# Kernel tuning notes

Hardware: AMD Instinct MI355X
Metric: run time of the kernel (lower is better)

The kernel has to match this reference:

```python
import jax, jax.numpy as jnp
import numpy as np

DROPOUT_P = 0.2
HEAD_SIZE = 64
EMBED = 1024


def setup_inputs() -> dict:
    key = jax.random.key(0)
    kx, kk, kq, kv = jax.random.split(key, 4)
    B, T = 4, 4096
    x = jax.random.normal(kx, (B, T, EMBED), dtype=jnp.float32)
    # torch Linear(embed, head, bias=False): y = x @ W.T with W [head, embed].
    # We store W_* as [embed, head] so projection is x @ W.
    scale = 1.0 / np.sqrt(EMBED)
    Wk = jax.random.uniform(kk, (EMBED, HEAD_SIZE), jnp.float32, -scale, scale)
    Wq = jax.random.uniform(kq, (EMBED, HEAD_SIZE), jnp.float32, -scale, scale)
    Wv = jax.random.uniform(kv, (EMBED, HEAD_SIZE), jnp.float32, -scale, scale)
    return {"x": x, "Wk": Wk, "Wq": Wq, "Wv": Wv}


def reference(x, Wk, Wq, Wv):
    # Projections: [B,T,E] @ [E,H] -> [B,T,H]
    k = jnp.einsum("bte,eh->bth", x, Wk)
    q = jnp.einsum("bte,eh->bth", x, Wq)
    v = jnp.einsum("bte,eh->bth", x, Wv)
    # Raw scaled scores, NO softmax: [B,T,T]
    w = jnp.einsum("bqh,bkh->bqk", q, k) * (HEAD_SIZE ** -0.5)
    # Dropout (training mode, inverted scaling) with a fixed key.
    keep = jax.random.bernoulli(jax.random.key(42), 1.0 - DROPOUT_P, w.shape)
    w = jnp.where(keep, w / (1.0 - DROPOUT_P), 0.0)
    # Weighted V sum: [B,T,T] @ [B,T,H] -> [B,T,H]
    return jnp.einsum("bqk,bkh->bqh", w, v)
```

## Files before the change

kernel.cpp:

```cpp
#include <hip/hip_runtime.h>


#define TB 4
#define TT 4096
#define TE 1024
#define TH 64
#define COMB_SCALE 0.15625f

typedef __bf16 bf16x8 __attribute__((ext_vector_type(8)));
typedef __bf16 bf16x4 __attribute__((ext_vector_type(4)));
typedef float  f32x4  __attribute__((ext_vector_type(4)));

#define ROTL(x, d) __builtin_amdgcn_alignbit((x), (x), 32u - (d))

__device__ __forceinline__ unsigned tf_bits(unsigned j) {
  const unsigned ks1 = 42u;
  const unsigned ks2 = 0x1BD11BDAu ^ 42u;
  unsigned x0 = 0u, x1 = j + ks1;
#define TF_RND(d) { x0 += x1; x1 = ROTL(x1, (d)); x1 ^= x0; }
  TF_RND(13u) TF_RND(15u) TF_RND(26u) TF_RND(6u)
  x0 += ks1; x1 += ks2 + 1u;
  TF_RND(17u) TF_RND(29u) TF_RND(16u) TF_RND(24u)
  x0 += ks2; x1 += 0u + 2u;
  TF_RND(13u) TF_RND(15u) TF_RND(26u) TF_RND(6u)
  x0 += 0u;  x1 += ks1 + 3u;
  TF_RND(17u) TF_RND(29u) TF_RND(16u) TF_RND(24u)
  x0 += ks1; x1 += ks2 + 4u;
  TF_RND(13u) TF_RND(15u) TF_RND(26u) TF_RND(6u)
  x0 += ks2; x1 += 0u + 5u;
#undef TF_RND
  return x0 ^ x1;
}

__device__ __forceinline__ unsigned tf_keepmask(unsigned j) {
  return tf_bits(j) < 3435974144u ? 0xFFFFFFFFu : 0u;
}

__global__ __launch_bounds__(256)
void prep_wt(const float* __restrict__ Wq, const float* __restrict__ Wk,
             const float* __restrict__ Wv, __bf16* __restrict__ WT)
{
  __shared__ float lds[64][65];
  const int wi = blockIdx.x >> 4;
  const int k0 = (blockIdx.x & 15) * 64;
  const float* W = (wi == 0) ? Wq : ((wi == 1) ? Wk : Wv);
  const int tid = threadIdx.x;
#pragma unroll
  for (int it = 0; it < 16; ++it) {
    const int idx = tid + it * 256;
    lds[idx >> 6][idx & 63] = W[(size_t)(k0 + (idx >> 6)) * TH + (idx & 63)];
  }
  __syncthreads();
#pragma unroll
  for (int it = 0; it < 16; ++it) {
    const int idx = tid + it * 256;
    const int n = idx >> 6, kk = idx & 63;
    WT[(size_t)(wi * TH + n) * TE + k0 + kk] = (__bf16)lds[kk][n];
  }
}

__global__ __launch_bounds__(256)
void proj_mfma(const float* __restrict__ x, const __bf16* __restrict__ WT,
               __bf16* __restrict__ qs, __bf16* __restrict__ ks,
               __bf16* __restrict__ vT)
{
  const int tid = threadIdx.x;
  const int w  = tid >> 6, l = tid & 63;
  const int l4 = l >> 4,  lm = l & 15;
  const int rh = w >> 1,  ch = w & 1;
  const int R  = blockIdx.x * 32 + rh * 16;

  const float*  xr = x  + (size_t)(R + lm) * TE;
  const __bf16* wt = WT + (size_t)(ch * 96 + lm) * TE;

  f32x4 acc[6];
#pragma unroll
  for (int t = 0; t < 6; ++t) acc[t] = (f32x4){0.f, 0.f, 0.f, 0.f};

  for (int k0 = 0; k0 < TE; k0 += 32) {
    const float4 u0 = *reinterpret_cast<const float4*>(xr + k0 + l4 * 8);
    const float4 u1 = *reinterpret_cast<const float4*>(xr + k0 + l4 * 8 + 4);
    bf16x8 am;
    am[0] = (__bf16)u0.x; am[1] = (__bf16)u0.y;
    am[2] = (__bf16)u0.z; am[3] = (__bf16)u0.w;
    am[4] = (__bf16)u1.x; am[5] = (__bf16)u1.y;
    am[6] = (__bf16)u1.z; am[7] = (__bf16)u1.w;
    bf16x8 bn[6];
#pragma unroll
    for (int t = 0; t < 6; ++t)
      bn[t] = *reinterpret_cast<const bf16x8*>(wt + (size_t)t * 16 * TE + k0 + l4 * 8);
#pragma unroll
    for (int t = 0; t < 6; ++t)
      acc[t] = __builtin_amdgcn_mfma_f32_16x16x32_bf16(am, bn[t], acc[t], 0, 0, 0);
  }

  const int row0 = R + l4 * 4;
#pragma unroll
  for (int t = 0; t < 6; ++t) {
    const int n = ch * 96 + t * 16 + lm;
    if (n < TH) {
#pragma unroll
      for (int r = 0; r < 4; ++r)
        qs[(size_t)(row0 + r) * TH + n] = (__bf16)(acc[t][r] * COMB_SCALE);
    } else if (n < 2 * TH) {
#pragma unroll
      for (int r = 0; r < 4; ++r)
        ks[(size_t)(row0 + r) * TH + (n - TH)] = (__bf16)acc[t][r];
    } else {
      bf16x4 vv;
#pragma unroll
      for (int r = 0; r < 4; ++r) vv[r] = (__bf16)acc[t][r];
      const int bb = row0 >> 12, trow = row0 & (TT - 1);
      *reinterpret_cast<bf16x4*>(
          vT + ((size_t)(bb * TH + (n - 2 * TH)) * TT + trow)) = vv;
    }
  }
}

__global__ __launch_bounds__(256, 4)
void attn_mfma(const __bf16* __restrict__ qs,
               const __bf16* __restrict__ ks,
               const __bf16* __restrict__ vT,
               float* __restrict__ out)
{
  __shared__ __bf16 S_lds[4][16 * 64];
  __shared__ float  Oex[3][16][TH + 4];

  const int tid = threadIdx.x;
  const int w   = tid >> 6;
  const int l   = tid & 63;
  const int l4  = l >> 4;
  const int lm  = l & 15;

  const int b     = blockIdx.x >> 8;
  const int qt16  = blockIdx.x & 255;
  const int qrow0 = qt16 * 16;
  const int kv0   = w * (TT / 4);

  const __bf16* qb = qs + ((size_t)b * TT + qrow0) * TH;
  const bf16x8 qf0 = *reinterpret_cast<const bf16x8*>(qb + (size_t)lm * TH + l4 * 8);
  const bf16x8 qf1 = *reinterpret_cast<const bf16x8*>(qb + (size_t)lm * TH + 32 + l4 * 8);

  const __bf16* kbp = ks + (size_t)b * TT * TH;
  const __bf16* vbp = vT + (size_t)b * TH * TT;

  f32x4 o_acc[4];
#pragma unroll
  for (int t = 0; t < 4; ++t) o_acc[t] = (f32x4){0.f, 0.f, 0.f, 0.f};

  const unsigned base0 = ((unsigned)(b * TT) + (unsigned)qrow0 + (unsigned)(l4 * 4)) * (unsigned)TT;
  const unsigned sw = (unsigned)((lm & 7) << 3);

  for (int kb = kv0; kb < kv0 + TT / 4; kb += 64) {
    bf16x8 kf[4][2];
#pragma unroll
    for (int t = 0; t < 4; ++t) {
      const __bf16* kr = kbp + (size_t)(kb + t * 16 + lm) * TH;
#pragma unroll
      for (int ss = 0; ss < 2; ++ss)
        kf[t][ss] = *reinterpret_cast<const bf16x8*>(kr + ss * 32 + l4 * 8);
    }
    bf16x8 vf[4][2];
#pragma unroll
    for (int t = 0; t < 4; ++t) {
      const __bf16* vr = vbp + (size_t)(t * 16 + lm) * TT + kb;
#pragma unroll
      for (int ss = 0; ss < 2; ++ss)
        vf[t][ss] = *reinterpret_cast<const bf16x8*>(vr + ss * 32 + l4 * 8);
    }

    unsigned km[4][4];
    const unsigned jcol = (unsigned)kb + (unsigned)lm;
#pragma unroll
    for (int t = 0; t < 4; ++t)
#pragma unroll
      for (int r = 0; r < 4; ++r)
        km[t][r] = tf_keepmask(base0 + (unsigned)(r << 12) + jcol + (unsigned)(t << 4));

    f32x4 sa[4];
#pragma unroll
    for (int t = 0; t < 4; ++t) {
      f32x4 c = {0.f, 0.f, 0.f, 0.f};
      c = __builtin_amdgcn_mfma_f32_16x16x32_bf16(qf0, kf[t][0], c, 0, 0, 0);
      c = __builtin_amdgcn_mfma_f32_16x16x32_bf16(qf1, kf[t][1], c, 0, 0, 0);
      sa[t] = c;
    }

#pragma unroll
    for (int t = 0; t < 4; ++t) {
#pragma unroll
      for (int r = 0; r < 4; ++r) {
        const unsigned sb = __float_as_uint(sa[t][r]) & km[t][r];
        const int row = l4 * 4 + r;
        const int col = t * 16 + lm;
        S_lds[w][row * 64 + (col ^ ((row & 7) << 3))] =
            (__bf16)__uint_as_float(sb);
      }
    }

    const bf16x8 af0 = *reinterpret_cast<const bf16x8*>(
        &S_lds[w][lm * 64 + ((unsigned)(l4 * 8) ^ sw)]);
    const bf16x8 af1 = *reinterpret_cast<const bf16x8*>(
        &S_lds[w][lm * 64 + ((unsigned)(32 + l4 * 8) ^ sw)]);

#pragma unroll
    for (int t = 0; t < 4; ++t) {
      o_acc[t] = __builtin_amdgcn_mfma_f32_16x16x32_bf16(af0, vf[t][0], o_acc[t], 0, 0, 0);
      o_acc[t] = __builtin_amdgcn_mfma_f32_16x16x32_bf16(af1, vf[t][1], o_acc[t], 0, 0, 0);
    }
  }

  if (w > 0) {
#pragma unroll
    for (int t = 0; t < 4; ++t)
#pragma unroll
      for (int r = 0; r < 4; ++r)
        Oex[w - 1][l4 * 4 + r][t * 16 + lm] = o_acc[t][r];
  }
  __syncthreads();
  if (w == 0) {
    float* outb = out + ((size_t)b * TT + qrow0) * TH;
#pragma unroll
    for (int t = 0; t < 4; ++t)
#pragma unroll
      for (int r = 0; r < 4; ++r) {
        const int row = l4 * 4 + r, col = t * 16 + lm;
        outb[(size_t)row * TH + col] = o_acc[t][r] + Oex[0][row][col] +
                                       Oex[1][row][col] + Oex[2][row][col];
      }
  }
}

extern "C" void kernel_launch(void* const* d_in, const int* in_sizes, int n_in,
                              void* d_out, int out_size, void* d_ws, size_t ws_size,
                              hipStream_t stream) {
  const float* x  = (const float*)d_in[0];
  const float* Wk = (const float*)d_in[1];
  const float* Wq = (const float*)d_in[2];
  const float* Wv = (const float*)d_in[3];
  float* outp = (float*)d_out;

  const size_t SZ = (size_t)TB * TT * TH;
  __bf16* q_ws  = (__bf16*)d_ws;
  __bf16* k_ws  = q_ws + SZ;
  __bf16* vT_ws = k_ws + SZ;
  __bf16* WT_ws = vT_ws + SZ;

  prep_wt<<<dim3(48), dim3(256), 0, stream>>>(Wq, Wk, Wv, WT_ws);
  proj_mfma<<<dim3(TB * TT / 32), dim3(256), 0, stream>>>(
      x, WT_ws, q_ws, k_ws, vT_ws);
  attn_mfma<<<dim3(TB * (TT / 16)), dim3(256), 0, stream>>>(
      q_ws, k_ws, vT_ws, outp);
}
```

Measured before the change: 203.1 us.

## Double-buffer K/V register loads in attention and prefetch in projection kernel

The attention kernel now ping-pongs between two register sets of K and V fragments, loading the next 64-key tile while the current one is processed, so global-load latency overlaps with the dropout hashing and MFMA work. The projection kernel is regridded to 16 rows per block with each of the four waves owning 48 output columns, which doubles the block count. It also software-prefetches the next x and W slice into registers. The gain in latency hiding costs more live registers, which under launch_bounds(256,4) could cause spills or lower occupancy.

```diff
diff --git a/kernel.cpp b/kernel.cpp
--- a/kernel.cpp
+++ b/kernel.cpp
@@ -32,10 +32,6 @@
   return x0 ^ x1;
 }
 
-__device__ __forceinline__ unsigned tf_keepmask(unsigned j) {
-  return tf_bits(j) < 3435974144u ? 0xFFFFFFFFu : 0u;
-}
-
 __global__ __launch_bounds__(256)
 void prep_wt(const float* __restrict__ Wq, const float* __restrict__ Wk,
              const float* __restrict__ Wv, __bf16* __restrict__ WT)
@@ -67,37 +63,49 @@
   const int tid = threadIdx.x;
   const int w  = tid >> 6, l = tid & 63;
   const int l4 = l >> 4,  lm = l & 15;
-  const int rh = w >> 1,  ch = w & 1;
-  const int R  = blockIdx.x * 32 + rh * 16;
+  const int R  = blockIdx.x * 16;
 
   const float*  xr = x  + (size_t)(R + lm) * TE;
-  const __bf16* wt = WT + (size_t)(ch * 96 + lm) * TE;
-
-  f32x4 acc[6];
-#pragma unroll
-  for (int t = 0; t < 6; ++t) acc[t] = (f32x4){0.f, 0.f, 0.f, 0.f};
+  const __bf16* wt = WT + (size_t)(w * 48 + lm) * TE;
+
+  f32x4 acc[3];
+#pragma unroll
+  for (int t = 0; t < 3; ++t) acc[t] = (f32x4){0.f, 0.f, 0.f, 0.f};
+
+  float4 u0 = *reinterpret_cast<const float4*>(xr + l4 * 8);
+  float4 u1 = *reinterpret_cast<const float4*>(xr + l4 * 8 + 4);
+  bf16x8 bnc[3];
+#pragma unroll
+  for (int t = 0; t < 3; ++t)
+    bnc[t] = *reinterpret_cast<const bf16x8*>(wt + (size_t)t * 16 * TE + l4 * 8);
 
   for (int k0 = 0; k0 < TE; k0 += 32) {
-    const float4 u0 = *reinterpret_cast<const float4*>(xr + k0 + l4 * 8);
-    const float4 u1 = *reinterpret_cast<const float4*>(xr + k0 + l4 * 8 + 4);
+    const int kp = (k0 + 32 < TE) ? (k0 + 32) : 0;
+    const float4 n0 = *reinterpret_cast<const float4*>(xr + kp + l4 * 8);
+    const float4 n1 = *reinterpret_cast<const float4*>(xr + kp + l4 * 8 + 4);
+    bf16x8 bnn[3];
+#pragma unroll
+    for (int t = 0; t < 3; ++t)
+      bnn[t] = *reinterpret_cast<const bf16x8*>(wt + (size_t)t * 16 * TE + kp + l4 * 8);
+
     bf16x8 am;
     am[0] = (__bf16)u0.x; am[1] = (__bf16)u0.y;
     am[2] = (__bf16)u0.z; am[3] = (__bf16)u0.w;
     am[4] = (__bf16)u1.x; am[5] = (__bf16)u1.y;
     am[6] = (__bf16)u1.z; am[7] = (__bf16)u1.w;
-    bf16x8 bn[6];
-#pragma unroll
-    for (int t = 0; t < 6; ++t)
-      bn[t] = *reinterpret_cast<const bf16x8*>(wt + (size_t)t * 16 * TE + k0 + l4 * 8);
-#pragma unroll
-    for (int t = 0; t < 6; ++t)
-      acc[t] = __builtin_amdgcn_mfma_f32_16x16x32_bf16(am, bn[t], acc[t], 0, 0, 0);
+#pragma unroll
+    for (int t = 0; t < 3; ++t)
+      acc[t] = __builtin_amdgcn_mfma_f32_16x16x32_bf16(am, bnc[t], acc[t], 0, 0, 0);
+
+    u0 = n0; u1 = n1;
+#pragma unroll
+    for (int t = 0; t < 3; ++t) bnc[t] = bnn[t];
   }
 
   const int row0 = R + l4 * 4;
 #pragma unroll
-  for (int t = 0; t < 6; ++t) {
-    const int n = ch * 96 + t * 16 + lm;
+  for (int t = 0; t < 3; ++t) {
+    const int n = w * 48 + t * 16 + lm;
     if (n < TH) {
 #pragma unroll
       for (int r = 0; r < 4; ++r)
@@ -151,8 +159,9 @@
   const unsigned base0 = ((unsigned)(b * TT) + (unsigned)qrow0 + (unsigned)(l4 * 4)) * (unsigned)TT;
   const unsigned sw = (unsigned)((lm & 7) << 3);
 
-  for (int kb = kv0; kb < kv0 + TT / 4; kb += 64) {
-    bf16x8 kf[4][2];
+  bf16x8 kfA[4][2], vfA[4][2], kfB[4][2], vfB[4][2];
+
+  auto loadkv = [&](bf16x8 (&kf)[4][2], bf16x8 (&vf)[4][2], int kb) {
 #pragma unroll
     for (int t = 0; t < 4; ++t) {
       const __bf16* kr = kbp + (size_t)(kb + t * 16 + lm) * TH;
@@ -160,7 +169,6 @@
       for (int ss = 0; ss < 2; ++ss)
         kf[t][ss] = *reinterpret_cast<const bf16x8*>(kr + ss * 32 + l4 * 8);
     }
-    bf16x8 vf[4][2];
 #pragma unroll
     for (int t = 0; t < 4; ++t) {
       const __bf16* vr = vbp + (size_t)(t * 16 + lm) * TT + kb;
@@ -168,14 +176,17 @@
       for (int ss = 0; ss < 2; ++ss)
         vf[t][ss] = *reinterpret_cast<const bf16x8*>(vr + ss * 32 + l4 * 8);
     }
-
+  };
+
+  auto work = [&](bf16x8 (&kf)[4][2], bf16x8 (&vf)[4][2], int kb) {
     unsigned km[4][4];
-    const unsigned jcol = (unsigned)kb + (unsigned)lm;
+    const unsigned j00 = base0 + (unsigned)kb + (unsigned)lm;
 #pragma unroll
     for (int t = 0; t < 4; ++t)
 #pragma unroll
       for (int r = 0; r < 4; ++r)
-        km[t][r] = tf_keepmask(base0 + (unsigned)(r << 12) + jcol + (unsigned)(t << 4));
+        km[t][r] = (tf_bits(j00 + (unsigned)((r << 12) + (t << 4))) <
+                    3435974144u) ? 0xFFFFFFFFu : 0u;
 
     f32x4 sa[4];
 #pragma unroll
@@ -208,6 +219,15 @@
       o_acc[t] = __builtin_amdgcn_mfma_f32_16x16x32_bf16(af0, vf[t][0], o_acc[t], 0, 0, 0);
       o_acc[t] = __builtin_amdgcn_mfma_f32_16x16x32_bf16(af1, vf[t][1], o_acc[t], 0, 0, 0);
     }
+  };
+
+  loadkv(kfA, vfA, kv0);
+#pragma unroll
+  for (int s = 0; s < 16; s += 2) {
+    loadkv(kfB, vfB, kv0 + (s + 1) * 64);
+    work(kfA, vfA, kv0 + s * 64);
+    if (s + 2 < 16) loadkv(kfA, vfA, kv0 + (s + 2) * 64);
+    work(kfB, vfB, kv0 + (s + 1) * 64);
   }
 
   if (w > 0) {
@@ -247,7 +267,7 @@
   __bf16* WT_ws = vT_ws + SZ;
 
   prep_wt<<<dim3(48), dim3(256), 0, stream>>>(Wq, Wk, Wv, WT_ws);
-  proj_mfma<<<dim3(TB * TT / 32), dim3(256), 0, stream>>>(
+  proj_mfma<<<dim3(TB * TT / 16), dim3(256), 0, stream>>>(
       x, WT_ws, q_ws, k_ws, vT_ws);
   attn_mfma<<<dim3(TB * (TT / 16)), dim3(256), 0, stream>>>(
       q_ws, k_ws, vT_ws, outp);
```

After: 262.2 us. 29.1% more time.

## Split projection K-dimension across waves with LDS reduction; raise MFMA wave priority

Applied to the files above, without the earlier changes.

The projection kernel now gives each block 16 rows and has each of its four waves cover a quarter of the embedding dimension for all 192 output columns. Partial sums are reduced through a large LDS buffer, which doubles the grid and fully unrolls a shorter K loop. The aim is more parallelism and better latency hiding for the x stream. Separately, the attention kernel raises wave priority around its MFMA sections with s_setprio so matrix work is scheduled ahead of the dropout hash ALU work of other waves. The costs are more LDS (about 50KB per block, which limits occupancy), higher register pressure, and an extra barrier.

```diff
diff --git a/kernel.cpp b/kernel.cpp
--- a/kernel.cpp
+++ b/kernel.cpp
@@ -59,25 +59,26 @@
   }
 }
 
-__global__ __launch_bounds__(256)
+__global__ __launch_bounds__(256, 3)
 void proj_mfma(const float* __restrict__ x, const __bf16* __restrict__ WT,
                __bf16* __restrict__ qs, __bf16* __restrict__ ks,
                __bf16* __restrict__ vT)
 {
+  __shared__ float red[4][16][196];
   const int tid = threadIdx.x;
   const int w  = tid >> 6, l = tid & 63;
   const int l4 = l >> 4,  lm = l & 15;
-  const int rh = w >> 1,  ch = w & 1;
-  const int R  = blockIdx.x * 32 + rh * 16;
-
-  const float*  xr = x  + (size_t)(R + lm) * TE;
-  const __bf16* wt = WT + (size_t)(ch * 96 + lm) * TE;
-
-  f32x4 acc[6];
-#pragma unroll
-  for (int t = 0; t < 6; ++t) acc[t] = (f32x4){0.f, 0.f, 0.f, 0.f};
-
-  for (int k0 = 0; k0 < TE; k0 += 32) {
+  const int R  = blockIdx.x * 16;
+
+  const float*  xr = x  + (size_t)(R + lm) * TE + w * 256;
+  const __bf16* wt = WT + (size_t)lm * TE + w * 256;
+
+  f32x4 acc[12];
+#pragma unroll
+  for (int t = 0; t < 12; ++t) acc[t] = (f32x4){0.f, 0.f, 0.f, 0.f};
+
+#pragma unroll
+  for (int k0 = 0; k0 < 256; k0 += 32) {
     const float4 u0 = *reinterpret_cast<const float4*>(xr + k0 + l4 * 8);
     const float4 u1 = *reinterpret_cast<const float4*>(xr + k0 + l4 * 8 + 4);
     bf16x8 am;
@@ -85,31 +86,44 @@
     am[2] = (__bf16)u0.z; am[3] = (__bf16)u0.w;
     am[4] = (__bf16)u1.x; am[5] = (__bf16)u1.y;
     am[6] = (__bf16)u1.z; am[7] = (__bf16)u1.w;
-    bf16x8 bn[6];
-#pragma unroll
-    for (int t = 0; t < 6; ++t)
+    bf16x8 bn[12];
+#pragma unroll
+    for (int t = 0; t < 12; ++t)
       bn[t] = *reinterpret_cast<const bf16x8*>(wt + (size_t)t * 16 * TE + k0 + l4 * 8);
 #pragma unroll
-    for (int t = 0; t < 6; ++t)
+    for (int t = 0; t < 12; ++t)
       acc[t] = __builtin_amdgcn_mfma_f32_16x16x32_bf16(am, bn[t], acc[t], 0, 0, 0);
   }
 
+#pragma unroll
+  for (int t = 0; t < 12; ++t)
+#pragma unroll
+    for (int r = 0; r < 4; ++r)
+      red[w][l4 * 4 + r][t * 16 + lm] = acc[t][r];
+  __syncthreads();
+
   const int row0 = R + l4 * 4;
 #pragma unroll
-  for (int t = 0; t < 6; ++t) {
-    const int n = ch * 96 + t * 16 + lm;
+  for (int t2 = 0; t2 < 3; ++t2) {
+    const int n = w * 48 + t2 * 16 + lm;
+    float v[4];
+#pragma unroll
+    for (int r = 0; r < 4; ++r) {
+      const int rr = l4 * 4 + r;
+      v[r] = red[0][rr][n] + red[1][rr][n] + red[2][rr][n] + red[3][rr][n];
+    }
     if (n < TH) {
 #pragma unroll
       for (int r = 0; r < 4; ++r)
-        qs[(size_t)(row0 + r) * TH + n] = (__bf16)(acc[t][r] * COMB_SCALE);
+        qs[(size_t)(row0 + r) * TH + n] = (__bf16)(v[r] * COMB_SCALE);
     } else if (n < 2 * TH) {
 #pragma unroll
       for (int r = 0; r < 4; ++r)
-        ks[(size_t)(row0 + r) * TH + (n - TH)] = (__bf16)acc[t][r];
+        ks[(size_t)(row0 + r) * TH + (n - TH)] = (__bf16)v[r];
     } else {
       bf16x4 vv;
 #pragma unroll
-      for (int r = 0; r < 4; ++r) vv[r] = (__bf16)acc[t][r];
+      for (int r = 0; r < 4; ++r) vv[r] = (__bf16)v[r];
       const int bb = row0 >> 12, trow = row0 & (TT - 1);
       *reinterpret_cast<bf16x4*>(
           vT + ((size_t)(bb * TH + (n - 2 * TH)) * TT + trow)) = vv;
@@ -177,6 +191,7 @@
       for (int r = 0; r < 4; ++r)
         km[t][r] = tf_keepmask(base0 + (unsigned)(r << 12) + jcol + (unsigned)(t << 4));
 
+    __builtin_amdgcn_s_setprio(1);
     f32x4 sa[4];
 #pragma unroll
     for (int t = 0; t < 4; ++t) {
@@ -185,6 +200,7 @@
       c = __builtin_amdgcn_mfma_f32_16x16x32_bf16(qf1, kf[t][1], c, 0, 0, 0);
       sa[t] = c;
     }
+    __builtin_amdgcn_s_setprio(0);
 
 #pragma unroll
     for (int t = 0; t < 4; ++t) {
@@ -203,11 +219,13 @@
     const bf16x8 af1 = *reinterpret_cast<const bf16x8*>(
         &S_lds[w][lm * 64 + ((unsigned)(32 + l4 * 8) ^ sw)]);
 
+    __builtin_amdgcn_s_setprio(1);
 #pragma unroll
     for (int t = 0; t < 4; ++t) {
       o_acc[t] = __builtin_amdgcn_mfma_f32_16x16x32_bf16(af0, vf[t][0], o_acc[t], 0, 0, 0);
       o_acc[t] = __builtin_amdgcn_mfma_f32_16x16x32_bf16(af1, vf[t][1], o_acc[t], 0, 0, 0);
     }
+    __builtin_amdgcn_s_setprio(0);
   }
 
   if (w > 0) {
@@ -247,7 +265,7 @@
   __bf16* WT_ws = vT_ws + SZ;
 
   prep_wt<<<dim3(48), dim3(256), 0, stream>>>(Wq, Wk, Wv, WT_ws);
-  proj_mfma<<<dim3(TB * TT / 32), dim3(256), 0, stream>>>(
+  proj_mfma<<<dim3(TB * TT / 16), dim3(256), 0, stream>>>(
       x, WT_ws, q_ws, k_ws, vT_ws);
   attn_mfma<<<dim3(TB * (TT / 16)), dim3(256), 0, stream>>>(
       q_ws, k_ws, vT_ws, outp);
```

New measurement: 191.5 us. -5.7%, faster.
